# Kernel optimization log

Measured on AMD Instinct MI355X. Metric: run time of the kernel, lower is better.

Reference implementation:

```python
import jax, jax.numpy as jnp
import numpy as np
from jax import lax


def setup_inputs() -> dict:
    key = jax.random.key(0)
    k1, k2 = jax.random.split(key)
    x = jax.random.normal(k1, (16, 256, 64, 64), dtype=jnp.float32)
    weight = jax.random.normal(k2, (1024, 256), dtype=jnp.float32)  # codebook (K, C)
    return {"x": x, "weight": weight}


def reference(x, weight):
    B, C, H, W = x.shape
    # (b c h w) -> (b h w) c
    xf = jnp.transpose(x, (0, 2, 3, 1)).reshape(-1, C)  # [N, C]
    d = (jnp.sum(xf * xf, axis=1, keepdims=True)
         + jnp.sum(weight * weight, axis=1)
         - 2.0 * (xf @ weight.T))
    indices = jnp.argmin(d, axis=1)  # [N], int
    z = weight[indices]  # [N, C] embedding lookup
    codebook_loss = jnp.mean((z - lax.stop_gradient(xf)) ** 2)
    commitment_loss = jnp.mean((xf - lax.stop_gradient(z)) ** 2)
    # straight-through estimator
    zq = xf + lax.stop_gradient(z - xf)
    zq = zq.reshape(B, H, W, C).transpose(0, 3, 1, 2)  # back to [B, C, H, W]
    sequence = indices.reshape(B, H, W)
    return zq, sequence, codebook_loss, commitment_loss
```

## Files before the change

kernel.cpp:

```cpp
#include <hip/hip_runtime.h>
#include <cfloat>
#include <climits>

#define B_   16
#define C_   256
#define K_   1024
#define HW_  4096
#define N_   (B_ * HW_)
#define CHW_ (C_ * HW_)

#define SEQ_OFF  16777216
#define LOSS_OFF (SEQ_OFF + N_)
#define WT_F    0
#define WN_F    262144
#define WNU_F   263168
#define WQ_F    264192
#define RLIST_F 395264
#define RCNT_F  526336
#define WMAX_F  526337

#define RL_CAP  131072
#define EPS_GAP 0.1f
#define XSCL    20.0f
#define XINV    0.05f
#define XOVF    6.3f

typedef int i32x4  __attribute__((ext_vector_type(4)));
typedef int i32x16 __attribute__((ext_vector_type(16)));

__device__ __forceinline__ int pack4b(int b0, int b1, int b2, int b3) {
    return (b0 & 0xFF) | ((b1 & 0xFF) << 8) | ((b2 & 0xFF) << 16) | ((b3 & 0xFF) << 24);
}

__global__ __launch_bounds__(256) void wmax_kernel(
    const float* __restrict__ w, unsigned* __restrict__ wmax_bits)
{
    const int tid = blockIdx.x * 256 + threadIdx.x;
    float mx = 0.f;
#pragma unroll
    for (int q = 0; q < 4; ++q) {
        const float4 v = reinterpret_cast<const float4*>(w)[tid * 4 + q];
        mx = fmaxf(mx, fmaxf(fmaxf(fabsf(v.x), fabsf(v.y)), fmaxf(fabsf(v.z), fabsf(v.w))));
    }
#pragma unroll
    for (int m = 1; m < 64; m <<= 1) mx = fmaxf(mx, __shfl_xor(mx, m, 64));
    if ((threadIdx.x & 63) == 0) atomicMax(wmax_bits, __float_as_uint(mx));
}

__global__ __launch_bounds__(256) void wprep_kernel(
    const float* __restrict__ w, const unsigned* __restrict__ wmax_bits,
    unsigned char* __restrict__ wq, float* __restrict__ w_t,
    float* __restrict__ wn, int* __restrict__ wnu)
{
    const int t = threadIdx.x;
    const int l = t & 63;
    const int k = blockIdx.x * 4 + (t >> 6);
    const float wmx = __uint_as_float(*wmax_bits);
    const float s   = 127.4f / wmx;
    const float d1  = wmx / 127.4f;
    const float sl  = s * 256.0f;

    const float4 v4 = *reinterpret_cast<const float4*>(w + (size_t)k * C_ + l * 4);
    float vv[4] = {v4.x, v4.y, v4.z, v4.w};
    float s2 = vv[0]*vv[0] + vv[1]*vv[1] + vv[2]*vv[2] + vv[3]*vv[3];
#pragma unroll
    for (int m = 1; m < 64; m <<= 1) s2 += __shfl_xor(s2, m, 64);

    const int chunk = k >> 5;
    const int col   = k & 31;
#pragma unroll
    for (int q = 0; q < 4; ++q) {
        const int c = l * 4 + q;
        const float v = vv[q];
        const int qh = (int)rintf(v * s);
        const float r = fmaf((float)qh, -d1, v);
        int ql = (int)rintf(r * sl);
        ql = max(-127, min(127, ql));
        const size_t off = (size_t)chunk * 16384 + (size_t)(c >> 5) * 1024
                         + (size_t)((c >> 4) & 1) * 512 + (size_t)col * 16 + (size_t)(c & 15);
        wq[off]        = (unsigned char)(qh & 0xFF);
        wq[off + 8192] = (unsigned char)(ql & 0xFF);
        w_t[(size_t)c * K_ + k] = v;
    }
    if (l == 0) {
        wn[k] = s2;
        wnu[k] = (int)rintf(s2 * (2560.0f / d1));
    }
}

__global__ __launch_bounds__(64, 2) void argmin_i8_kernel(
    const float* __restrict__ x, const unsigned char* __restrict__ wq,
    const int* __restrict__ wnu, const unsigned* __restrict__ wmax_bits,
    float* __restrict__ seq, int* __restrict__ rlist, int* __restrict__ rcount)
{
    const int l = threadIdx.x;
    const int col = l & 31;
    const int khalf = l >> 5;
    const int nb = blockIdx.x;
    const int b  = nb >> 7;
    const int hw0 = (nb & 127) << 5;
    const float* xb = x + (size_t)b * CHW_ + hw0 + col;

    i32x4 ah8[8], al8[8];
    float mx = 0.f;
#pragma unroll
    for (int cc = 0; cc < 8; ++cc) {
        int qh[16], ql[16];
#pragma unroll
        for (int j = 0; j < 16; ++j) {
            const float v = xb[(size_t)(cc * 32 + khalf * 16 + j) * HW_];
            mx = fmaxf(mx, fabsf(v));
            int h = (int)rintf(v * XSCL);
            h = max(-127, min(127, h));
            const float r = fmaf((float)h, -XINV, v);
            int lo = (int)rintf(r * (XSCL * 256.0f));
            lo = max(-127, min(127, lo));
            qh[j] = h; ql[j] = lo;
        }
        ah8[cc] = (i32x4){ pack4b(qh[0],qh[1],qh[2],qh[3]),   pack4b(qh[4],qh[5],qh[6],qh[7]),
                           pack4b(qh[8],qh[9],qh[10],qh[11]), pack4b(qh[12],qh[13],qh[14],qh[15]) };
        al8[cc] = (i32x4){ pack4b(ql[0],ql[1],ql[2],ql[3]),   pack4b(ql[4],ql[5],ql[6],ql[7]),
                           pack4b(ql[8],ql[9],ql[10],ql[11]), pack4b(ql[12],ql[13],ql[14],ql[15]) };
    }

    mx = fmaxf(mx, __shfl_xor(mx, 32, 64));
    if (khalf == 0 && mx > XOVF) {
        const int pos = atomicAdd(rcount, 1);
        if (pos < RL_CAP) rlist[pos] = b * HW_ + hw0 + col;
    }

    const float wmx = __uint_as_float(*wmax_bits);
    const int eps_u = (int)(32614.4f / wmx);

    int m1p[16], m2p[16];
#pragma unroll
    for (int r = 0; r < 16; ++r) { m1p[r] = INT_MAX; m2p[r] = INT_MAX; }

#pragma unroll 1
    for (int ch = 0; ch < 32; ++ch) {
        const unsigned char* base = wq + (size_t)ch * 16384 + l * 16;
        const int wnu_l = wnu[ch * 32 + col];

        i32x16 aH, aX;
#pragma unroll
        for (int r = 0; r < 16; ++r) { aH[r] = 0; aX[r] = 0; }

#pragma unroll
        for (int half = 0; half < 2; ++half) {
            i32x4 bh[4], bl[4];
#pragma unroll
            for (int q = 0; q < 4; ++q) {
                const int ks = half * 4 + q;
                bh[q] = *reinterpret_cast<const i32x4*>(base + ks * 1024);
                bl[q] = *reinterpret_cast<const i32x4*>(base + 8192 + ks * 1024);
            }
#pragma unroll
            for (int q = 0; q < 4; ++q) {
                const int ks = half * 4 + q;
                aH = __builtin_amdgcn_mfma_i32_32x32x32_i8(ah8[ks], bh[q], aH, 0, 0, 0);
                aX = __builtin_amdgcn_mfma_i32_32x32x32_i8(ah8[ks], bl[q], aX, 0, 0, 0);
                aX = __builtin_amdgcn_mfma_i32_32x32x32_i8(al8[ks], bh[q], aX, 0, 0, 0);
            }
        }

#pragma unroll
        for (int r = 0; r < 16; ++r) {
            const int T  = (aH[r] << 8) + aX[r];
            const int D  = wnu_l - T;
            const int Dp = (D & ~31) | ch;
            m2p[r] = min(m2p[r], max(m1p[r], Dp));
            m1p[r] = min(m1p[r], Dp);
        }
    }

    int k1[16];
#pragma unroll
    for (int r = 0; r < 16; ++r) k1[r] = ((m1p[r] & 31) << 5) | col;
#pragma unroll
    for (int mask = 1; mask <= 16; mask <<= 1) {
#pragma unroll
        for (int r = 0; r < 16; ++r) {
            const int om1 = __shfl_xor(m1p[r], mask, 64);
            const int ok1 = __shfl_xor(k1[r],  mask, 64);
            const int om2 = __shfl_xor(m2p[r], mask, 64);
            const int nm2 = min(min(m2p[r], om2), max(m1p[r], om1));
            const bool lt = om1 < m1p[r] || (om1 == m1p[r] && ok1 < k1[r]);
            m1p[r] = lt ? om1 : m1p[r];
            k1[r]  = lt ? ok1 : k1[r];
            m2p[r] = nm2;
        }
    }

    if (col == 0) {
#pragma unroll
        for (int r = 0; r < 16; ++r) {
            const int row_local = (r & 3) + 8 * (r >> 2) + 4 * khalf;
            const int n = b * HW_ + hw0 + row_local;
            seq[n] = (float)k1[r];
            if (m2p[r] - m1p[r] < eps_u) {
                const int pos = atomicAdd(rcount, 1);
                if (pos < RL_CAP) rlist[pos] = n;
            }
        }
    }
}

__global__ __launch_bounds__(256) void rescue_kernel(
    const float* __restrict__ x, const float* __restrict__ w_t,
    const float* __restrict__ wnorm, const int* __restrict__ rlist,
    const int* __restrict__ rcount, float* __restrict__ seq)
{
    __shared__ float xr[C_];
    __shared__ float bvs[4];
    __shared__ int   bis[4];
    const int t = threadIdx.x;
    const int cnt = min(*rcount, RL_CAP);
    for (int ii = blockIdx.x; ii < cnt; ii += gridDim.x) {
        const int n = rlist[ii];
        const int b = n >> 12, hw = n & 4095;
        xr[t] = x[(size_t)b * CHW_ + (size_t)t * HW_ + hw];
        __syncthreads();
        float best = FLT_MAX; int bidx = 0;
#pragma unroll
        for (int q = 0; q < 4; ++q) {
            const int k = t + q * 256;
            float acc = 0.f;
            for (int c = 0; c < C_; ++c) acc = fmaf(xr[c], w_t[(size_t)c * K_ + k], acc);
            const float d = wnorm[k] - 2.f * acc;
            if (d < best || (d == best && k < bidx)) { best = d; bidx = k; }
        }
#pragma unroll
        for (int mask = 1; mask < 64; mask <<= 1) {
            const float ov = __shfl_xor(best, mask, 64);
            const int   oi = __shfl_xor(bidx, mask, 64);
            if (ov < best || (ov == best && oi < bidx)) { best = ov; bidx = oi; }
        }
        if ((t & 63) == 0) { bvs[t >> 6] = best; bis[t >> 6] = bidx; }
        __syncthreads();
        if (t == 0) {
            float bv = bvs[0]; int bi = bis[0];
#pragma unroll
            for (int w2 = 1; w2 < 4; ++w2)
                if (bvs[w2] < bv || (bvs[w2] == bv && bis[w2] < bi)) { bv = bvs[w2]; bi = bis[w2]; }
            seq[n] = (float)bi;
        }
        __syncthreads();
    }
}

__global__ __launch_bounds__(256) void gather_kernel(
    const float* __restrict__ x, const float* __restrict__ w,
    const float* __restrict__ seqf, float* __restrict__ zq,
    double* __restrict__ loss_acc)
{
    __shared__ float ws[C_ * 64];
    const int t   = threadIdx.x;
    const int nb  = blockIdx.x;
    const int b   = nb >> 6;
    const int hw0 = (nb & 63) << 6;
    {
        const int j = t >> 2, q = t & 3;
        const int idx = (int)seqf[b * HW_ + hw0 + j];
        const float* wrow = w + (size_t)idx * C_ + q * 64;
#pragma unroll
        for (int m = 0; m < 16; ++m) {
            const float4 v = *reinterpret_cast<const float4*>(wrow + m * 4);
            const int c = q * 64 + m * 4;
            ws[(c + 0) * 64 + j] = v.x;
            ws[(c + 1) * 64 + j] = v.y;
            ws[(c + 2) * 64 + j] = v.z;
            ws[(c + 3) * 64 + j] = v.w;
        }
    }
    __syncthreads();
    const int r  = t & 63;
    const int cg = t >> 6;
    const float* xb = x  + (size_t)b * CHW_ + hw0;
    float*       zb = zq + (size_t)b * CHW_ + hw0;
    float lsum = 0.f;
#pragma unroll 4
    for (int cc = 0; cc < 64; ++cc) {
        const int c = cg * 64 + cc;
        const float xv = xb[(size_t)c * HW_ + r];
        const float d  = ws[c * 64 + r] - xv;
        zb[(size_t)c * HW_ + r] = xv + d;
        lsum += d * d;
    }
#pragma unroll
    for (int off = 32; off >= 1; off >>= 1) lsum += __shfl_down(lsum, off, 64);
    __syncthreads();
    if ((t & 63) == 0) ws[t >> 6] = lsum;
    __syncthreads();
    if (t == 0)
        atomicAdd(loss_acc, (double)(ws[0] + ws[1] + ws[2] + ws[3]));
}

__global__ void finalize_kernel(const double* __restrict__ acc, float* __restrict__ loss_out)
{
    const double s = *acc;
    const float m = (float)(s / (double)((size_t)N_ * C_));
    loss_out[0] = m;
    loss_out[1] = m;
}

extern "C" void kernel_launch(void* const* d_in, const int* in_sizes, int n_in,
                              void* d_out, int out_size, void* d_ws, size_t ws_size,
                              hipStream_t stream)
{
    (void)in_sizes; (void)n_in; (void)out_size; (void)d_ws; (void)ws_size;
    const float* x = (const float*)d_in[0];
    const float* w = (const float*)d_in[1];
    float* out = (float*)d_out;

    float*         w_t    = out + WT_F;
    float*         wn     = out + WN_F;
    int*           wnu    = (int*)(out + WNU_F);
    unsigned char* wq     = (unsigned char*)(out + WQ_F);
    int*           rlist  = (int*)(out + RLIST_F);
    int*           rcount = (int*)(out + RCNT_F);
    unsigned*      wmaxb  = (unsigned*)(out + WMAX_F);
    float*         seq    = out + SEQ_OFF;
    double*        loss_acc = (double*)(out + LOSS_OFF);

    hipMemsetAsync((void*)wmaxb, 0, 4, stream);
    hipMemsetAsync((void*)rcount, 0, 4, stream);
    wmax_kernel<<<64, 256, 0, stream>>>(w, wmaxb);
    wprep_kernel<<<256, 256, 0, stream>>>(w, wmaxb, wq, w_t, wn, wnu);
    argmin_i8_kernel<<<2048, 64, 0, stream>>>(x, wq, wnu, wmaxb, seq, rlist, rcount);
    rescue_kernel<<<1024, 256, 0, stream>>>(x, w_t, wn, rlist, rcount, seq);
    hipMemsetAsync((char*)d_out + (size_t)LOSS_OFF * 4, 0, 8, stream);
    gather_kernel<<<1024, 256, 0, stream>>>(x, w, seq, out, loss_acc);
    finalize_kernel<<<1, 1, 0, stream>>>(loss_acc, out + LOSS_OFF);
}
```

Baseline: 193.2 us.

## Switch argmin GEMM from 32x32x32 to 16x16x64 int8 MFMA tiles

Rebuilds the int8 codebook distance kernel around the 16x16x64 i8 MFMA instead of 32x32x32. Each wave now covers 32 rows as two 16-row tiles against 16-code chunks (64 chunks instead of 32), and the quantized weight layout, packing of the chunk index into the low bits, and shuffle reduction are changed to match. The aim is higher MFMA throughput and smaller accumulators, with fewer per-lane min updates and shuffles. The cost is twice as many loop iterations and B-operand loads per chunk, plus six independent accumulator chains.

New measurement: 191.5 us. Within noise of the previous version (-0.9%).

```diff
diff --git a/kernel.cpp b/kernel.cpp
--- a/kernel.cpp
+++ b/kernel.cpp
@@ -25,8 +25,7 @@
 #define XINV    0.05f
 #define XOVF    6.3f
 
-typedef int i32x4  __attribute__((ext_vector_type(4)));
-typedef int i32x16 __attribute__((ext_vector_type(16)));
+typedef int i32x4 __attribute__((ext_vector_type(4)));
 
 __device__ __forceinline__ int pack4b(int b0, int b1, int b2, int b3) {
     return (b0 & 0xFF) | ((b1 & 0xFF) << 8) | ((b2 & 0xFF) << 16) | ((b3 & 0xFF) << 24);
@@ -66,8 +65,8 @@
 #pragma unroll
     for (int m = 1; m < 64; m <<= 1) s2 += __shfl_xor(s2, m, 64);
 
-    const int chunk = k >> 5;
-    const int col   = k & 31;
+    const int chunk = k >> 4;
+    const int col   = k & 15;
 #pragma unroll
     for (int q = 0; q < 4; ++q) {
         const int c = l * 4 + q;
@@ -76,10 +75,10 @@
         const float r = fmaf((float)qh, -d1, v);
         int ql = (int)rintf(r * sl);
         ql = max(-127, min(127, ql));
-        const size_t off = (size_t)chunk * 16384 + (size_t)(c >> 5) * 1024
-                         + (size_t)((c >> 4) & 1) * 512 + (size_t)col * 16 + (size_t)(c & 15);
+        const size_t off = (size_t)chunk * 8192 + (size_t)(c >> 6) * 1024
+                         + (size_t)((c >> 4) & 3) * 256 + (size_t)col * 16 + (size_t)(c & 15);
         wq[off]        = (unsigned char)(qh & 0xFF);
-        wq[off + 8192] = (unsigned char)(ql & 0xFF);
+        wq[off + 4096] = (unsigned char)(ql & 0xFF);
         w_t[(size_t)c * K_ + k] = v;
     }
     if (l == 0) {
@@ -93,113 +92,134 @@
     const int* __restrict__ wnu, const unsigned* __restrict__ wmax_bits,
     float* __restrict__ seq, int* __restrict__ rlist, int* __restrict__ rcount)
 {
-    const int l = threadIdx.x;
-    const int col = l & 31;
-    const int khalf = l >> 5;
-    const int nb = blockIdx.x;
-    const int b  = nb >> 7;
+    const int l   = threadIdx.x;
+    const int col = l & 15;
+    const int kg  = l >> 4;
+    const int nb  = blockIdx.x;
+    const int b   = nb >> 7;
     const int hw0 = (nb & 127) << 5;
-    const float* xb = x + (size_t)b * CHW_ + hw0 + col;
-
-    i32x4 ah8[8], al8[8];
-    float mx = 0.f;
-#pragma unroll
-    for (int cc = 0; cc < 8; ++cc) {
-        int qh[16], ql[16];
-#pragma unroll
-        for (int j = 0; j < 16; ++j) {
-            const float v = xb[(size_t)(cc * 32 + khalf * 16 + j) * HW_];
-            mx = fmaxf(mx, fabsf(v));
-            int h = (int)rintf(v * XSCL);
-            h = max(-127, min(127, h));
-            const float r = fmaf((float)h, -XINV, v);
-            int lo = (int)rintf(r * (XSCL * 256.0f));
-            lo = max(-127, min(127, lo));
-            qh[j] = h; ql[j] = lo;
-        }
-        ah8[cc] = (i32x4){ pack4b(qh[0],qh[1],qh[2],qh[3]),   pack4b(qh[4],qh[5],qh[6],qh[7]),
-                           pack4b(qh[8],qh[9],qh[10],qh[11]), pack4b(qh[12],qh[13],qh[14],qh[15]) };
-        al8[cc] = (i32x4){ pack4b(ql[0],ql[1],ql[2],ql[3]),   pack4b(ql[4],ql[5],ql[6],ql[7]),
-                           pack4b(ql[8],ql[9],ql[10],ql[11]), pack4b(ql[12],ql[13],ql[14],ql[15]) };
-    }
-
-    mx = fmaxf(mx, __shfl_xor(mx, 32, 64));
-    if (khalf == 0 && mx > XOVF) {
-        const int pos = atomicAdd(rcount, 1);
-        if (pos < RL_CAP) rlist[pos] = b * HW_ + hw0 + col;
+    const float* xb = x + (size_t)b * CHW_ + hw0;
+
+    i32x4 ah[2][4], al[2][4];
+    float mxr[2] = {0.f, 0.f};
+#pragma unroll
+    for (int t = 0; t < 2; ++t) {
+        const int row = t * 16 + col;
+#pragma unroll
+        for (int s = 0; s < 4; ++s) {
+            int qh[16], ql[16];
+#pragma unroll
+            for (int j = 0; j < 16; ++j) {
+                const float v = xb[(size_t)(s * 64 + kg * 16 + j) * HW_ + row];
+                mxr[t] = fmaxf(mxr[t], fabsf(v));
+                int h = (int)rintf(v * XSCL);
+                h = max(-127, min(127, h));
+                const float r = fmaf((float)h, -XINV, v);
+                int lo = (int)rintf(r * (XSCL * 256.0f));
+                lo = max(-127, min(127, lo));
+                qh[j] = h; ql[j] = lo;
+            }
+            ah[t][s] = (i32x4){ pack4b(qh[0],qh[1],qh[2],qh[3]),   pack4b(qh[4],qh[5],qh[6],qh[7]),
+                                pack4b(qh[8],qh[9],qh[10],qh[11]), pack4b(qh[12],qh[13],qh[14],qh[15]) };
+            al[t][s] = (i32x4){ pack4b(ql[0],ql[1],ql[2],ql[3]),   pack4b(ql[4],ql[5],ql[6],ql[7]),
+                                pack4b(ql[8],ql[9],ql[10],ql[11]), pack4b(ql[12],ql[13],ql[14],ql[15]) };
+        }
+    }
+
+#pragma unroll
+    for (int t = 0; t < 2; ++t) {
+        mxr[t] = fmaxf(mxr[t], __shfl_xor(mxr[t], 16, 64));
+        mxr[t] = fmaxf(mxr[t], __shfl_xor(mxr[t], 32, 64));
+        if (kg == 0 && mxr[t] > XOVF) {
+            const int pos = atomicAdd(rcount, 1);
+            if (pos < RL_CAP) rlist[pos] = b * HW_ + hw0 + t * 16 + col;
+        }
     }
 
     const float wmx = __uint_as_float(*wmax_bits);
     const int eps_u = (int)(32614.4f / wmx);
 
-    int m1p[16], m2p[16];
-#pragma unroll
-    for (int r = 0; r < 16; ++r) { m1p[r] = INT_MAX; m2p[r] = INT_MAX; }
+    int m1p[2][4], m2p[2][4];
+#pragma unroll
+    for (int t = 0; t < 2; ++t)
+#pragma unroll
+        for (int i = 0; i < 4; ++i) { m1p[t][i] = INT_MAX; m2p[t][i] = INT_MAX; }
 
 #pragma unroll 1
-    for (int ch = 0; ch < 32; ++ch) {
-        const unsigned char* base = wq + (size_t)ch * 16384 + l * 16;
-        const int wnu_l = wnu[ch * 32 + col];
-
-        i32x16 aH, aX;
-#pragma unroll
-        for (int r = 0; r < 16; ++r) { aH[r] = 0; aX[r] = 0; }
-
-#pragma unroll
-        for (int half = 0; half < 2; ++half) {
-            i32x4 bh[4], bl[4];
-#pragma unroll
-            for (int q = 0; q < 4; ++q) {
-                const int ks = half * 4 + q;
-                bh[q] = *reinterpret_cast<const i32x4*>(base + ks * 1024);
-                bl[q] = *reinterpret_cast<const i32x4*>(base + 8192 + ks * 1024);
+    for (int ch = 0; ch < 64; ++ch) {
+        const unsigned char* base = wq + (size_t)ch * 8192 + l * 16;
+        const int wnu_l = wnu[ch * 16 + col];
+
+        i32x4 bh[4], bl[4];
+#pragma unroll
+        for (int s = 0; s < 4; ++s) {
+            bh[s] = *reinterpret_cast<const i32x4*>(base + s * 1024);
+            bl[s] = *reinterpret_cast<const i32x4*>(base + 4096 + s * 1024);
+        }
+
+        i32x4 aH0 = {0,0,0,0}, aH1 = {0,0,0,0};
+        i32x4 aXa0 = {0,0,0,0}, aXb0 = {0,0,0,0};
+        i32x4 aXa1 = {0,0,0,0}, aXb1 = {0,0,0,0};
+#pragma unroll
+        for (int s = 0; s < 4; ++s) {
+            aH0  = __builtin_amdgcn_mfma_i32_16x16x64_i8(ah[0][s], bh[s], aH0, 0, 0, 0);
+            aH1  = __builtin_amdgcn_mfma_i32_16x16x64_i8(ah[1][s], bh[s], aH1, 0, 0, 0);
+            aXa0 = __builtin_amdgcn_mfma_i32_16x16x64_i8(ah[0][s], bl[s], aXa0, 0, 0, 0);
+            aXb0 = __builtin_amdgcn_mfma_i32_16x16x64_i8(al[0][s], bh[s], aXb0, 0, 0, 0);
+            aXa1 = __builtin_amdgcn_mfma_i32_16x16x64_i8(ah[1][s], bl[s], aXa1, 0, 0, 0);
+            aXb1 = __builtin_amdgcn_mfma_i32_16x16x64_i8(al[1][s], bh[s], aXb1, 0, 0, 0);
+        }
+
+#pragma unroll
+        for (int i = 0; i < 4; ++i) {
+            const int T0  = (aH0[i] << 8) + aXa0[i] + aXb0[i];
+            const int D0  = wnu_l - T0;
+            const int Dp0 = (D0 & ~63) | ch;
+            m2p[0][i] = min(m2p[0][i], max(m1p[0][i], Dp0));
+            m1p[0][i] = min(m1p[0][i], Dp0);
+            const int T1  = (aH1[i] << 8) + aXa1[i] + aXb1[i];
+            const int D1  = wnu_l - T1;
+            const int Dp1 = (D1 & ~63) | ch;
+            m2p[1][i] = min(m2p[1][i], max(m1p[1][i], Dp1));
+            m1p[1][i] = min(m1p[1][i], Dp1);
+        }
+    }
+
+    int k1[2][4];
+#pragma unroll
+    for (int t = 0; t < 2; ++t)
+#pragma unroll
+        for (int i = 0; i < 4; ++i) k1[t][i] = ((m1p[t][i] & 63) << 4) | col;
+#pragma unroll
+    for (int mask = 1; mask <= 8; mask <<= 1) {
+#pragma unroll
+        for (int t = 0; t < 2; ++t) {
+#pragma unroll
+            for (int i = 0; i < 4; ++i) {
+                const int om1 = __shfl_xor(m1p[t][i], mask, 64);
+                const int ok1 = __shfl_xor(k1[t][i],  mask, 64);
+                const int om2 = __shfl_xor(m2p[t][i], mask, 64);
+                const int nm2 = min(min(m2p[t][i], om2), max(m1p[t][i], om1));
+                const bool lt = om1 < m1p[t][i] || (om1 == m1p[t][i] && ok1 < k1[t][i]);
+                m1p[t][i] = lt ? om1 : m1p[t][i];
+                k1[t][i]  = lt ? ok1 : k1[t][i];
+                m2p[t][i] = nm2;
             }
-#pragma unroll
-            for (int q = 0; q < 4; ++q) {
-                const int ks = half * 4 + q;
-                aH = __builtin_amdgcn_mfma_i32_32x32x32_i8(ah8[ks], bh[q], aH, 0, 0, 0);
-                aX = __builtin_amdgcn_mfma_i32_32x32x32_i8(ah8[ks], bl[q], aX, 0, 0, 0);
-                aX = __builtin_amdgcn_mfma_i32_32x32x32_i8(al8[ks], bh[q], aX, 0, 0, 0);
-            }
-        }
-
-#pragma unroll
-        for (int r = 0; r < 16; ++r) {
-            const int T  = (aH[r] << 8) + aX[r];
-            const int D  = wnu_l - T;
-            const int Dp = (D & ~31) | ch;
-            m2p[r] = min(m2p[r], max(m1p[r], Dp));
-            m1p[r] = min(m1p[r], Dp);
-        }
-    }
-
-    int k1[16];
-#pragma unroll
-    for (int r = 0; r < 16; ++r) k1[r] = ((m1p[r] & 31) << 5) | col;
-#pragma unroll
-    for (int mask = 1; mask <= 16; mask <<= 1) {
-#pragma unroll
-        for (int r = 0; r < 16; ++r) {
-            const int om1 = __shfl_xor(m1p[r], mask, 64);
-            const int ok1 = __shfl_xor(k1[r],  mask, 64);
-            const int om2 = __shfl_xor(m2p[r], mask, 64);
-            const int nm2 = min(min(m2p[r], om2), max(m1p[r], om1));
-            const bool lt = om1 < m1p[r] || (om1 == m1p[r] && ok1 < k1[r]);
-            m1p[r] = lt ? om1 : m1p[r];
-            k1[r]  = lt ? ok1 : k1[r];
-            m2p[r] = nm2;
         }
     }
 
     if (col == 0) {
 #pragma unroll
-        for (int r = 0; r < 16; ++r) {
-            const int row_local = (r & 3) + 8 * (r >> 2) + 4 * khalf;
-            const int n = b * HW_ + hw0 + row_local;
-            seq[n] = (float)k1[r];
-            if (m2p[r] - m1p[r] < eps_u) {
-                const int pos = atomicAdd(rcount, 1);
-                if (pos < RL_CAP) rlist[pos] = n;
+        for (int t = 0; t < 2; ++t) {
+#pragma unroll
+            for (int i = 0; i < 4; ++i) {
+                const int row_local = t * 16 + kg * 4 + i;
+                const int n = b * HW_ + hw0 + row_local;
+                seq[n] = (float)k1[t][i];
+                if (m2p[t][i] - m1p[t][i] < eps_u) {
+                    const int pos = atomicAdd(rcount, 1);
+                    if (pos < RL_CAP) rlist[pos] = n;
+                }
             }
         }
     }
```
